# Optimization experiments

Measured on AMD Instinct MI355X. Metric: run time of the kernel, lower is better.

## Reference

```python
import jax, jax.numpy as jnp
import numpy as np

NUM_LEVELS = 4
RADIUS = 4


def _bilinear_zeros(img, x, y):
    """Bilinear sample img (N,H,W) at absolute pixel coords x,y (N,S,S),
    zeros padding outside, matching torch grid_sample(align_corners=True,
    padding_mode='zeros') with absolute->normalized->absolute roundtrip."""
    N, H, W = img.shape
    x0 = jnp.floor(x); y0 = jnp.floor(y)
    x1 = x0 + 1.0;     y1 = y0 + 1.0
    wx1 = x - x0; wx0 = 1.0 - wx1
    wy1 = y - y0; wy0 = 1.0 - wy1
    flat = img.reshape(N, H * W)

    def gather(xi, yi):
        valid = (xi >= 0) & (xi <= W - 1) & (yi >= 0) & (yi <= H - 1)
        xc = jnp.clip(xi, 0, W - 1).astype(jnp.int32)
        yc = jnp.clip(yi, 0, H - 1).astype(jnp.int32)
        idx = (yc * W + xc).reshape(N, -1)
        v = jnp.take_along_axis(flat, idx, axis=1).reshape(xi.shape)
        return jnp.where(valid, v, jnp.zeros((), img.dtype))

    return (wy0 * wx0 * gather(x0, y0) + wy0 * wx1 * gather(x1, y0)
            + wy1 * wx0 * gather(x0, y1) + wy1 * wx1 * gather(x1, y1))


def _avg_pool2(v):
    N, H, W = v.shape
    return v.reshape(N, H // 2, 2, W // 2, 2).mean(axis=(2, 4))


def setup_inputs() -> dict:
    key = jax.random.key(0)
    k1, k2, k3 = jax.random.split(key, 3)
    B, M, C, H, W = 2, 4096, 256, 64, 64
    fmap1 = jax.random.normal(k1, (B, M, C), dtype=jnp.float32)
    fmap2 = jax.random.normal(k2, (B, C, H, W), dtype=jnp.float32)
    u = jax.random.uniform(k3, (B, M, 2), dtype=jnp.float32)
    centroids_coords = u * jnp.array([W - 1, H - 1], dtype=jnp.float32)
    return {"fmap1": fmap1, "fmap2": fmap2, "centroids_coords": centroids_coords}


def reference(fmap1, fmap2, centroids_coords):
    B, M, C = fmap1.shape
    _, _, H, W = fmap2.shape
    side = 2 * RADIUS + 1

    # correlation volume: (B, M, H, W) -> (B*M, H, W)
    corr = jnp.einsum('bmc,bchw->bmhw', fmap1, fmap2).reshape(B * M, H, W)

    d = jnp.arange(-RADIUS, RADIUS + 1, dtype=centroids_coords.dtype)
    di, dj = jnp.meshgrid(d, d, indexing='ij')
    delta = jnp.stack([di, dj], axis=-1)  # (S, S, 2): ch0 = x-offset, ch1 = y-offset

    c = centroids_coords.reshape(B * M, 1, 1, 2)
    vol = corr
    feats = []
    for lvl in range(NUM_LEVELS):
        sc = c + delta                        # (B*M, S, S, 2)
        sampled = _bilinear_zeros(vol, sc[..., 0], sc[..., 1])
        feats.append(sampled.reshape(B, M, side * side))
        c = c / 2.0
        if lvl < NUM_LEVELS - 1:
            vol = _avg_pool2(vol)
    # (B, M, num_levels*S*S) -> (B, out_channels, M)
    return jnp.concatenate(feats, axis=-1).transpose(0, 2, 1)
```

## Files before the change

### kernel.cpp

```cpp
#include <hip/hip_runtime.h>
#include <stdint.h>
#include <stddef.h>

static constexpr int Bb = 2;
static constexpr int Mq = 4096;
static constexpr int Cc = 256;
static constexpr int Hh = 64, Ww = 64;
static constexpr int Np = Hh * Ww;
static constexpr int NL1 = 1024;
static constexpr int RAD = 4;
static constexpr int SIDE = 2 * RAD + 1;
static constexpr int KPL = SIDE * SIDE;
static constexpr int NLVL = 4;
static constexpr int KTOT = NLVL * KPL;

static constexpr size_t L1BUF_B  = 0;
static constexpr size_t WINBUF_B = (size_t)Bb * Mq * 1024 * 2;
static constexpr size_t ABF_B    = WINBUF_B + (size_t)Bb * Mq * 100 * 4;
static constexpr size_t BT_B     = ABF_B + (size_t)Bb * Mq * Cc * 2;
static constexpr size_t B1T_B    = BT_B + (size_t)Bb * Np * Cc * 2;

typedef float floatx4 __attribute__((ext_vector_type(4)));
typedef short shortx8 __attribute__((ext_vector_type(8)));

union BfPack {
    shortx8 v;
    unsigned short u[8];
};

__device__ __forceinline__ unsigned short f2bf(float f) {
    unsigned int x = __float_as_uint(f);
    x += 0x7fffu + ((x >> 16) & 1u);
    return (unsigned short)(x >> 16);
}

__device__ __forceinline__ float bf2f(unsigned short u) {
    return __uint_as_float((unsigned int)u << 16);
}

__device__ __forceinline__ void gll16(const void* g, void* l) {
    __builtin_amdgcn_global_load_lds(
        (const __attribute__((address_space(1))) unsigned int*)g,
        (__attribute__((address_space(3))) unsigned int*)l, 16, 0, 0);
}

__global__ __launch_bounds__(256)
void cvt_kernel(const float* __restrict__ f1, const float* __restrict__ f2,
                unsigned short* __restrict__ Abf, unsigned short* __restrict__ Bt,
                unsigned short* __restrict__ B1t)
{
    __shared__ float tile[64 * 132];
    const int tid = threadIdx.x;
    if (blockIdx.x < 1024) {
        const int t = blockIdx.x * 256 + tid;
        const float4 v0 = *(const float4*)(f1 + (size_t)t * 8);
        const float4 v1 = *(const float4*)(f1 + (size_t)t * 8 + 4);
        BfPack p;
        p.u[0] = f2bf(v0.x); p.u[1] = f2bf(v0.y);
        p.u[2] = f2bf(v0.z); p.u[3] = f2bf(v0.w);
        p.u[4] = f2bf(v1.x); p.u[5] = f2bf(v1.y);
        p.u[6] = f2bf(v1.z); p.u[7] = f2bf(v1.w);
        *(shortx8*)(Abf + (size_t)t * 8) = p.v;
        return;
    }
    const int bid  = blockIdx.x - 1024;
    const int b    = bid >> 7;
    const int cblk = (bid >> 5) & 3;
    const int y1   = bid & 31;

#pragma unroll
    for (int i = 0; i < 8; ++i) {
        const int v  = i * 256 + tid;
        const int c  = v >> 5;
        const int f4 = v & 31;
        *(float4*)&tile[c * 132 + f4 * 4] =
            *(const float4*)&f2[((size_t)(b * Cc + cblk * 64 + c)) * Np + y1 * 128 + f4 * 4];
    }
    __syncthreads();

#pragma unroll
    for (int i = 0; i < 4; ++i) {
        const int w  = i * 256 + tid;
        const int rp = w >> 3;
        const int cg = w & 7;
        BfPack p;
#pragma unroll
        for (int u = 0; u < 8; ++u)
            p.u[u] = f2bf(tile[(cg * 8 + u) * 132 + rp]);
        *(shortx8*)&Bt[((size_t)(b * Np + y1 * 128 + rp)) * Cc + cblk * 64 + cg * 8] = p.v;
    }

    {
        const int x1 = tid >> 3;
        const int cg = tid & 7;
        BfPack p;
#pragma unroll
        for (int u = 0; u < 8; ++u) {
            const int c = cg * 8 + u;
            const float v = 0.25f * (tile[c * 132 + 2 * x1]      + tile[c * 132 + 2 * x1 + 1]
                                   + tile[c * 132 + 64 + 2 * x1] + tile[c * 132 + 64 + 2 * x1 + 1]);
            p.u[u] = f2bf(v);
        }
        *(shortx8*)&B1t[((size_t)(b * NL1 + y1 * 32 + x1)) * Cc + cblk * 64 + cg * 8] = p.v;
    }
}

__global__ __launch_bounds__(256)
void win_kernel(const unsigned short* __restrict__ Abf,
                const unsigned short* __restrict__ Bt,
                const float* __restrict__ cent,
                float* __restrict__ winbuf)
{
    const int tid  = threadIdx.x;
    const int wave = tid >> 6;
    const int lane = tid & 63;
    const int h    = lane >> 5;
    const int cl   = lane & 31;
    const size_t gq = (size_t)blockIdx.x * 4 + wave;
    const int b = (int)(gq >> 12);

    float a[8];
    {
        BfPack ap;
        ap.v = *(const shortx8*)&Abf[gq * Cc + cl * 8];
#pragma unroll
        for (int u = 0; u < 8; ++u) a[u] = bf2f(ap.u[u]);
    }

    const float cx = cent[gq * 2 + 0];
    const float cy = cent[gq * 2 + 1];
    const int x0 = (int)floorf(cx) - RAD;
    const int y0 = (int)floorf(cy) - RAD;
    const int xlo = x0 > 0 ? x0 : 0;
    const int xhim = x0 + 9 < Ww - 1 ? x0 + 9 : Ww - 1;
    const int npx = xhim - xlo + 1;
    const int wxbase = xlo - x0;

    for (int wy = 0; wy < 10; ++wy) {
        const int y = y0 + wy;
        if ((unsigned)y > 63u) continue;
        const unsigned short* bp =
            Bt + ((size_t)(b * Np) + (size_t)(y * Ww + xlo)) * Cc + cl * 8;

        float acc0 = 0.f, acc1 = 0.f, acc2 = 0.f, acc3 = 0.f, acc4 = 0.f;
#pragma unroll
        for (int it = 0; it < 5; ++it) {
            const int p = it * 2 + h;
            if (p < npx) {
                BfPack bv;
                bv.v = *(const shortx8*)&bp[p * Cc];
                float s = 0.f;
#pragma unroll
                for (int u = 0; u < 8; ++u)
                    s = fmaf(a[u], bf2f(bv.u[u]), s);
                if (it == 0) acc0 += s;
                else if (it == 1) acc1 += s;
                else if (it == 2) acc2 += s;
                else if (it == 3) acc3 += s;
                else acc4 += s;
            }
        }
#pragma unroll
        for (int m = 16; m >= 1; m >>= 1) {
            acc0 += __shfl_xor(acc0, m);
            acc1 += __shfl_xor(acc1, m);
            acc2 += __shfl_xor(acc2, m);
            acc3 += __shfl_xor(acc3, m);
            acc4 += __shfl_xor(acc4, m);
        }
        float val = acc0;
        val = (cl == 1) ? acc1 : val;
        val = (cl == 2) ? acc2 : val;
        val = (cl == 3) ? acc3 : val;
        val = (cl == 4) ? acc4 : val;
        const int p = cl * 2 + h;
        if (cl < 5 && p < npx)
            winbuf[gq * 100 + wy * 10 + wxbase + p] = val;
    }
}

__global__ __launch_bounds__(256)
void l1_gemm_kernel(const unsigned short* __restrict__ Abf,
                    const unsigned short* __restrict__ B1t,
                    unsigned short* __restrict__ l1buf)
{
    __shared__ union {
        unsigned short stage[2][2][128 * 32];
        float corrT[32 * 132];
    } sm;

    const int b    = blockIdx.z;
    const int bm0  = blockIdx.y * 128;
    const int bn0  = blockIdx.x * 128;
    const int tid  = threadIdx.x;
    const int lane = tid & 63;
    const int wave = tid >> 6;
    const int lane15 = lane & 15;
    const int quad   = lane >> 4;
    const int wm = (wave >> 1) * 64;
    const int wn = (wave & 1) * 64;

    const int lrow = lane >> 2;
    const int lkg  = (((lane & 3) ^ ((lrow >> 1) & 3))) * 8;
    const unsigned short* aptr = Abf + (size_t)(b * Mq + bm0 + wave * 16 + lrow) * Cc + lkg;
    const unsigned short* bptr = B1t + (size_t)(b * NL1 + bn0 + wave * 16 + lrow) * Cc + lkg;

    floatx4 acc[4][4];
#pragma unroll
    for (int i = 0; i < 4; ++i)
#pragma unroll
        for (int j = 0; j < 4; ++j)
            acc[i][j] = floatx4{0.0f, 0.0f, 0.0f, 0.0f};

    gll16(aptr,           &sm.stage[0][0][wave * 512]);
    gll16(aptr + 64 * Cc, &sm.stage[0][0][2048 + wave * 512]);
    gll16(bptr,           &sm.stage[0][1][wave * 512]);
    gll16(bptr + 64 * Cc, &sm.stage[0][1][2048 + wave * 512]);

    const int rq = (quad ^ ((lane15 >> 1) & 3)) * 8;

    for (int k0 = 0; k0 < 8; ++k0) {
        __syncthreads();
        if (k0 < 7) {
            const int nb = (k0 + 1) & 1;
            const int ko = (k0 + 1) * 32;
            gll16(aptr + ko,           &sm.stage[nb][0][wave * 512]);
            gll16(aptr + 64 * Cc + ko, &sm.stage[nb][0][2048 + wave * 512]);
            gll16(bptr + ko,           &sm.stage[nb][1][wave * 512]);
            gll16(bptr + 64 * Cc + ko, &sm.stage[nb][1][2048 + wave * 512]);
        }
        const unsigned short* la = sm.stage[k0 & 1][0];
        const unsigned short* lb = sm.stage[k0 & 1][1];
        shortx8 af[4], bf[4];
#pragma unroll
        for (int i = 0; i < 4; ++i)
            af[i] = *(const shortx8*)&la[(wm + i * 16 + lane15) * 32 + rq];
#pragma unroll
        for (int j = 0; j < 4; ++j)
            bf[j] = *(const shortx8*)&lb[(wn + j * 16 + lane15) * 32 + rq];
#pragma unroll
        for (int i = 0; i < 4; ++i)
#pragma unroll
            for (int j = 0; j < 4; ++j)
                acc[i][j] = __builtin_amdgcn_mfma_f32_16x16x32_bf16(
                    af[i], bf[j], acc[i][j], 0, 0, 0);
    }

    float* corrT = sm.corrT;
    const int row = tid >> 3;
    const int g   = tid & 7;
#pragma unroll
    for (int c = 0; c < 4; ++c) {
        __syncthreads();
        if ((wave >> 1) == (c >> 1)) {
#pragma unroll
            for (int ii = 0; ii < 2; ++ii) {
                const int i = 2 * (c & 1) + ii;
#pragma unroll
                for (int j = 0; j < 4; ++j) {
#pragma unroll
                    for (int reg = 0; reg < 4; ++reg) {
                        const int rl = ii * 16 + quad * 4 + reg;
                        const int n  = wn + j * 16 + lane15;
                        corrT[rl * 132 + n] = acc[i][j][reg];
                    }
                }
            }
        }
        __syncthreads();

        const size_t gq = (size_t)(b * Mq + bm0 + 32 * c + row);
        const float* T = &corrT[row * 132];
        BfPack p0, p1;
#pragma unroll
        for (int u = 0; u < 8; ++u) {
            p0.u[u] = f2bf(T[g * 16 + u]);
            p1.u[u] = f2bf(T[g * 16 + 8 + u]);
        }
        *(shortx8*)&l1buf[gq * 1024 + bn0 + g * 16]     = p0.v;
        *(shortx8*)&l1buf[gq * 1024 + bn0 + g * 16 + 8] = p1.v;
    }
}

__global__ __launch_bounds__(256)
void pyr_sample_kernel(const float* __restrict__ cent,
                       const unsigned short* __restrict__ l1buf,
                       const float* __restrict__ winbuf,
                       float* __restrict__ out)
{
    __shared__ float l1[8][1024];
    __shared__ float l2[8][256];
    __shared__ float l3[8][64];
    __shared__ float win0[8][100];
    __shared__ float qcx[8], qcy[8];
    __shared__ int   qx0[8], qy0[8];

    const int tid = threadIdx.x;
    const int b   = blockIdx.x >> 9;
    const int m0  = (blockIdx.x & 511) * 8;
    const size_t gq0 = (size_t)(b * Mq + m0);

    if (tid < 8) {
        const float cx = cent[(gq0 + tid) * 2 + 0];
        const float cy = cent[(gq0 + tid) * 2 + 1];
        qcx[tid] = cx; qcy[tid] = cy;
        qx0[tid] = (int)floorf(cx) - RAD;
        qy0[tid] = (int)floorf(cy) - RAD;
    }

#pragma unroll
    for (int it = 0; it < 4; ++it) {
        const int v = it * 256 + tid;
        const int q = v >> 7;
        const int o = v & 127;
        BfPack p;
        p.v = *(const shortx8*)&l1buf[(gq0 + q) * 1024 + o * 8];
#pragma unroll
        for (int u = 0; u < 8; ++u)
            l1[q][o * 8 + u] = bf2f(p.u[u]);
    }
    if (tid < 200) {
        const int q = tid / 25;
        const int o = tid - q * 25;
        *(float4*)&win0[q][o * 4] = *(const float4*)&winbuf[(gq0 + q) * 100 + o * 4];
    }
    __syncthreads();

#pragma unroll
    for (int i = 0; i < 8; ++i) {
        const int idx = i * 256 + tid;
        const int q = idx >> 8;
        const int c = idx & 255;
        const int cy2 = c >> 4, cx2 = c & 15;
        const float* s = &l1[q][(2 * cy2) * 32 + 2 * cx2];
        l2[q][c] = 0.25f * (s[0] + s[1] + s[32] + s[33]);
    }
    __syncthreads();
#pragma unroll
    for (int i = 0; i < 2; ++i) {
        const int idx = i * 256 + tid;
        const int q = idx >> 6;
        const int c = idx & 63;
        const int cy3 = c >> 3, cx3 = c & 7;
        const float* s = &l2[q][(2 * cy3) * 16 + 2 * cx3];
        l3[q][c] = 0.25f * (s[0] + s[1] + s[16] + s[17]);
    }
    __syncthreads();

    for (int i = 0; i < 11; ++i) {
        const int idx = i * 256 + tid;
        if (idx >= KTOT * 8) break;
        const int q  = idx & 7;
        const int kk = idx >> 3;
        const int lvl = kk / KPL;
        const int r   = kk - lvl * KPL;
        const int di  = r / SIDE;
        const int dj  = r - di * SIDE;

        const int w = Ww >> lvl;
        const float scale = 1.0f / (float)(1 << lvl);
        const float x = qcx[q] * scale + (float)(di - RAD);
        const float y = qcy[q] * scale + (float)(dj - RAD);

        const float x0f = floorf(x), y0f = floorf(y);
        const float wx1 = x - x0f, wx0 = 1.0f - wx1;
        const float wy1 = y - y0f, wy0 = 1.0f - wy1;
        const float fmx = (float)(w - 1);
        const bool vx0 = (x0f >= 0.0f) && (x0f <= fmx);
        const bool vx1 = (x0f + 1.0f >= 0.0f) && (x0f + 1.0f <= fmx);
        const bool vy0 = (y0f >= 0.0f) && (y0f <= fmx);
        const bool vy1 = (y0f + 1.0f >= 0.0f) && (y0f + 1.0f <= fmx);

        const int ix0 = (int)x0f, iy0 = (int)y0f;

        const float* buf;
        int stride, ox, oy;
        if (lvl == 0)      { buf = win0[q]; stride = 10; ox = qx0[q]; oy = qy0[q]; }
        else if (lvl == 1) { buf = l1[q];   stride = 32; ox = 0; oy = 0; }
        else if (lvl == 2) { buf = l2[q];   stride = 16; ox = 0; oy = 0; }
        else               { buf = l3[q];   stride =  8; ox = 0; oy = 0; }

        const int cx0 = ix0 - ox, cx1 = ix0 + 1 - ox;
        const int cy0r = iy0 - oy, cy1r = iy0 + 1 - oy;
        const float g00 = (vx0 && vy0) ? buf[cy0r * stride + cx0] : 0.0f;
        const float g10 = (vx1 && vy0) ? buf[cy0r * stride + cx1] : 0.0f;
        const float g01 = (vx0 && vy1) ? buf[cy1r * stride + cx0] : 0.0f;
        const float g11 = (vx1 && vy1) ? buf[cy1r * stride + cx1] : 0.0f;

        out[((size_t)b * KTOT + kk) * Mq + m0 + q] =
            wy0 * (wx0 * g00 + wx1 * g10) + wy1 * (wx0 * g01 + wx1 * g11);
    }
}

extern "C" void kernel_launch(void* const* d_in, const int* in_sizes, int n_in,
                              void* d_out, int out_size, void* d_ws, size_t ws_size,
                              hipStream_t stream)
{
    const float* fmap1 = (const float*)d_in[0];
    const float* fmap2 = (const float*)d_in[1];
    const float* cent  = (const float*)d_in[2];
    char* ws = (char*)d_ws;
    unsigned short* l1buf = (unsigned short*)(ws + L1BUF_B);
    float* winbuf = (float*)(ws + WINBUF_B);
    unsigned short* Abf = (unsigned short*)(ws + ABF_B);
    unsigned short* Bt  = (unsigned short*)(ws + BT_B);
    unsigned short* B1t = (unsigned short*)(ws + B1T_B);
    float* out = (float*)d_out;

    cvt_kernel<<<1280, 256, 0, stream>>>(fmap1, fmap2, Abf, Bt, B1t);

    win_kernel<<<Bb * Mq / 4, 256, 0, stream>>>(Abf, Bt, cent, winbuf);

    dim3 ggrid(NL1 / 128, Mq / 128, Bb);
    l1_gemm_kernel<<<ggrid, 256, 0, stream>>>(Abf, B1t, l1buf);

    const int nblk = Bb * Mq / 8;
    pyr_sample_kernel<<<nblk, 256, 0, stream>>>(cent, l1buf, winbuf, out);
}
```

Measured before the change: 135.4 us.

## Bin queries by spatial cell and stage shared Bt region in LDS

win_kernel is reorganized so that each block owns one 4x4 spatial cell per batch. The block collects the queries whose centroid falls in that cell into a shared list via an atomic counter. It then loads the 13x13-pixel, 256-channel bf16 neighbourhood of fmap2 into LDS once, and each wave computes window correlations for its queries from LDS. Before, every query re-read its own 10x10 window from global memory. The change cuts repeated L2/global traffic. In exchange, every block scans all centroids, uses about 86 KB of LDS at 512 threads (low occupancy), risks load imbalance across cells, and silently drops queries beyond 128 per cell.

```diff
diff --git a/kernel.cpp b/kernel.cpp
--- a/kernel.cpp
+++ b/kernel.cpp
@@ -105,77 +105,116 @@
     }
 }
 
-__global__ __launch_bounds__(256)
+__global__ __launch_bounds__(512)
 void win_kernel(const unsigned short* __restrict__ Abf,
                 const unsigned short* __restrict__ Bt,
                 const float* __restrict__ cent,
                 float* __restrict__ winbuf)
 {
+    __shared__ unsigned short reg[13 * 13 * 256];
+    __shared__ int qlist[128];
+    __shared__ int qcnt;
+
     const int tid  = threadIdx.x;
+    const int b    = blockIdx.x >> 8;
+    const int cell = blockIdx.x & 255;
+    const int biny = cell >> 4;
+    const int binx = cell & 15;
+    const int xmin = (4 * binx - 4) > 0 ? (4 * binx - 4) : 0;
+    const int ymin = (4 * biny - 4) > 0 ? (4 * biny - 4) : 0;
+    const int xmax = (4 * binx + 8) < 63 ? (4 * binx + 8) : 63;
+    const int ymax = (4 * biny + 8) < 63 ? (4 * biny + 8) : 63;
+    const int rh = ymax - ymin + 1;
+    const int rw = xmax - xmin + 1;
+
+    if (tid == 0) qcnt = 0;
+    __syncthreads();
+
+#pragma unroll
+    for (int i = 0; i < 8; ++i) {
+        const int m = i * 512 + tid;
+        const float2 cc = *(const float2*)&cent[((size_t)b * Mq + m) * 2];
+        const int qbx = ((int)floorf(cc.x)) >> 2;
+        const int qby = ((int)floorf(cc.y)) >> 2;
+        if (qbx == binx && qby == biny) {
+            const int idx = atomicAdd(&qcnt, 1);
+            if (idx < 128) qlist[idx] = m;
+        }
+    }
+
+    const int rw32 = rw * 32;
+    for (int ry = 0; ry < rh; ++ry) {
+        if (tid < rw32) {
+            const size_t g = ((size_t)(b * Np) + (size_t)((ymin + ry) * Ww + xmin)) * Cc
+                           + (size_t)tid * 8;
+            *(shortx8*)&reg[(ry * 13) * 256 + tid * 8] = *(const shortx8*)&Bt[g];
+        }
+    }
+    __syncthreads();
+
+    const int cnt = qcnt < 128 ? qcnt : 128;
     const int wave = tid >> 6;
     const int lane = tid & 63;
     const int h    = lane >> 5;
     const int cl   = lane & 31;
-    const size_t gq = (size_t)blockIdx.x * 4 + wave;
-    const int b = (int)(gq >> 12);
-
-    float a[8];
-    {
-        BfPack ap;
-        ap.v = *(const shortx8*)&Abf[gq * Cc + cl * 8];
-#pragma unroll
-        for (int u = 0; u < 8; ++u) a[u] = bf2f(ap.u[u]);
-    }
-
-    const float cx = cent[gq * 2 + 0];
-    const float cy = cent[gq * 2 + 1];
-    const int x0 = (int)floorf(cx) - RAD;
-    const int y0 = (int)floorf(cy) - RAD;
-    const int xlo = x0 > 0 ? x0 : 0;
-    const int xhim = x0 + 9 < Ww - 1 ? x0 + 9 : Ww - 1;
-    const int npx = xhim - xlo + 1;
-    const int wxbase = xlo - x0;
-
-    for (int wy = 0; wy < 10; ++wy) {
-        const int y = y0 + wy;
-        if ((unsigned)y > 63u) continue;
-        const unsigned short* bp =
-            Bt + ((size_t)(b * Np) + (size_t)(y * Ww + xlo)) * Cc + cl * 8;
-
-        float acc0 = 0.f, acc1 = 0.f, acc2 = 0.f, acc3 = 0.f, acc4 = 0.f;
-#pragma unroll
-        for (int it = 0; it < 5; ++it) {
-            const int p = it * 2 + h;
-            if (p < npx) {
-                BfPack bv;
-                bv.v = *(const shortx8*)&bp[p * Cc];
-                float s = 0.f;
-#pragma unroll
-                for (int u = 0; u < 8; ++u)
-                    s = fmaf(a[u], bf2f(bv.u[u]), s);
-                if (it == 0) acc0 += s;
-                else if (it == 1) acc1 += s;
-                else if (it == 2) acc2 += s;
-                else if (it == 3) acc3 += s;
-                else acc4 += s;
+
+    for (int qi = wave; qi < cnt; qi += 8) {
+        const int m = qlist[qi];
+        const size_t gq = (size_t)b * Mq + m;
+
+        float a[8];
+        {
+            BfPack ap;
+            ap.v = *(const shortx8*)&Abf[gq * Cc + cl * 8];
+#pragma unroll
+            for (int u = 0; u < 8; ++u) a[u] = bf2f(ap.u[u]);
+        }
+        const float2 cc = *(const float2*)&cent[gq * 2];
+        const int x0 = (int)floorf(cc.x) - RAD;
+        const int y0 = (int)floorf(cc.y) - RAD;
+
+        for (int wy = 0; wy < 10; ++wy) {
+            const int y = y0 + wy;
+            if ((unsigned)y > 63u) continue;
+            const int rybase = ((y - ymin) * 13 - xmin) * 256;
+
+            float acc0 = 0.f, acc1 = 0.f, acc2 = 0.f, acc3 = 0.f, acc4 = 0.f;
+#pragma unroll
+            for (int it = 0; it < 5; ++it) {
+                const int p = it * 2 + h;
+                const int x = x0 + p;
+                if ((unsigned)x <= 63u) {
+                    BfPack bv;
+                    bv.v = *(const shortx8*)&reg[rybase + x * 256 + cl * 8];
+                    float s = 0.f;
+#pragma unroll
+                    for (int u = 0; u < 8; ++u)
+                        s = fmaf(a[u], bf2f(bv.u[u]), s);
+                    if (it == 0) acc0 += s;
+                    else if (it == 1) acc1 += s;
+                    else if (it == 2) acc2 += s;
+                    else if (it == 3) acc3 += s;
+                    else acc4 += s;
+                }
             }
-        }
-#pragma unroll
-        for (int m = 16; m >= 1; m >>= 1) {
-            acc0 += __shfl_xor(acc0, m);
-            acc1 += __shfl_xor(acc1, m);
-            acc2 += __shfl_xor(acc2, m);
-            acc3 += __shfl_xor(acc3, m);
-            acc4 += __shfl_xor(acc4, m);
-        }
-        float val = acc0;
-        val = (cl == 1) ? acc1 : val;
-        val = (cl == 2) ? acc2 : val;
-        val = (cl == 3) ? acc3 : val;
-        val = (cl == 4) ? acc4 : val;
-        const int p = cl * 2 + h;
-        if (cl < 5 && p < npx)
-            winbuf[gq * 100 + wy * 10 + wxbase + p] = val;
+#pragma unroll
+            for (int mm = 16; mm >= 1; mm >>= 1) {
+                acc0 += __shfl_xor(acc0, mm);
+                acc1 += __shfl_xor(acc1, mm);
+                acc2 += __shfl_xor(acc2, mm);
+                acc3 += __shfl_xor(acc3, mm);
+                acc4 += __shfl_xor(acc4, mm);
+            }
+            float val = acc0;
+            val = (cl == 1) ? acc1 : val;
+            val = (cl == 2) ? acc2 : val;
+            val = (cl == 3) ? acc3 : val;
+            val = (cl == 4) ? acc4 : val;
+            const int p = cl * 2 + h;
+            const int x = x0 + p;
+            if (cl < 5 && (unsigned)x <= 63u)
+                winbuf[gq * 100 + wy * 10 + p] = val;
+        }
     }
 }
 
@@ -409,7 +448,7 @@
 
     cvt_kernel<<<1280, 256, 0, stream>>>(fmap1, fmap2, Abf, Bt, B1t);
 
-    win_kernel<<<Bb * Mq / 4, 256, 0, stream>>>(Abf, Bt, cent, winbuf);
+    win_kernel<<<Bb * 256, 512, 0, stream>>>(Abf, Bt, cent, winbuf);
 
     dim3 ggrid(NL1 / 128, Mq / 128, Bb);
     l1_gemm_kernel<<<ggrid, 256, 0, stream>>>(Abf, B1t, l1buf);
```

Measured after the change: 172.7 us. 1.28x slower.
